# Optimization experiments

Measured on AMD Instinct MI355X. Metric: run time of the kernel, lower is better.

## Reference

```python
import jax, jax.numpy as jnp
import numpy as np

N = 512        # input image side (== n after rounding, cor = n//2)
N_DET = 512
N_SPAN = 3
N_ANGLES_INIT = 1024
BATCH = 16
C = 1


def _splineB3(x2, r):
    sizex = len(x2)
    x2 = x2 - (x2[-1] + x2[0]) / 2
    stepx = x2[1] - x2[0]
    ri = int(np.ceil(2 * r))
    r = r * stepx
    c = int(np.ceil((sizex + 1) / 2.0))
    x2c = x2[c - 1]
    x = x2[c - ri - 1:c + ri]
    d = np.abs(x - x2c) / r
    B3 = np.zeros_like(x)
    for ix in range(-ri, ri + 1):
        i = ix + ri
        if d[i] < 1:
            B3[i] = (3 * d[i] ** 3 - 6 * d[i] ** 2 + 4) / 6
        elif d[i] < 2:
            B3[i] = (-d[i] ** 3 + 6 * d[i] ** 2 - 12 * d[i] + 8) / 6
    B3f = np.zeros_like(x2)
    B3f[c - ri - 1:c + ri] = B3
    return B3f


def _precompute():
    beta = np.pi / N_SPAN
    n = N  # ceil((512+0)/16)*16 == 512 since cor == n//2
    n_det = N_DET
    os_angles = int(max(round(3.0 * n / 2 / N_ANGLES_INIT), 1))  # == 1
    n_angles = os_angles * N_ANGLES_INIT
    angles = np.arange(n_angles) * np.pi / n_angles - beta / 2
    s = np.linspace(-1, 1, n_det)
    a_R = np.sin(beta / 2) / (1 + np.sin(beta / 2))
    a_m = (np.cos(beta / 2) - np.sin(beta / 2)) / (1 + np.sin(beta / 2))
    t = np.linspace(-np.pi / 2, np.pi / 2, 1000)
    w = a_R * np.cos(t) + (1 - a_R) + 1j * a_R * np.sin(t)
    g = np.nanmax(np.log(np.abs(w)) + np.log(np.cos(beta / 2 - np.arctan2(w.imag, w.real))))
    n_th = n_det
    n_rho = 2 * n_det
    d_th = 2 * beta / n_th
    d_rho = (g - np.log(a_m)) / n_rho
    th_lp = np.arange(-n_th / 2, n_th / 2) * d_th
    rho_lp = np.arange(-n_rho, 0) * d_rho
    b3_th = np.fft.fft(np.fft.ifftshift(_splineB3(th_lp, 1)))
    b3_rho = np.fft.fft(np.fft.ifftshift(_splineB3(rho_lp, 1)))
    b3_com = np.outer(b3_rho, b3_th)
    # ---- zeta coefficients (vectorized over k_rho) ----
    n_th_large = 4 * n_th
    k_rho = np.arange(-n_rho / 2, n_rho / 2, dtype='float32')
    th_sp_large = np.arange(-n_th_large / 2, n_th_large / 2) / n_th_large * beta * 2
    h = np.ones(n_th_large)
    correcting = 1 + np.array([-216254335, 679543284, -1412947389, 2415881496, -3103579086,
                               2939942400, -2023224114, 984515304, -321455811, 63253516,
                               -5675265]) / 958003200.0
    correcting[0] = 2 * (correcting[0] - 0.5)
    h[0] *= correcting[0]
    for j in range(1, len(correcting)):
        h[j] *= correcting[j]
        h[-j] *= correcting[j]
    expo = -2 * np.pi * 1j * k_rho / (g - np.log(a_m)) - 1
    fcosa = np.cos(th_sp_large)[None, :].astype('complex128') ** expo[:, None]
    fZ = np.fft.fftshift(np.fft.fft(np.fft.fftshift(h[None, :] * fcosa, axes=-1), axis=-1), axes=-1)
    fZ = fZ[:, n_th_large // 2 - n_th // 2: n_th_large // 2 + n_th // 2] * (th_sp_large[1] - th_sp_large[0])
    fZ[0] = 0
    fZ[:, 0] = 0
    zeta = np.fft.fftshift(fZ)
    const = np.sqrt(n_det * os_angles / n_angles) * np.pi / 4 / a_R / np.sqrt(2)
    zeta = zeta[:, :n_th // 2 + 1] * const
    zeta = zeta / b3_com[:, :n_th // 2 + 1]  # cubic interp prefilter compensation
    # ---- cartesian -> log-polar gather indices (floor, per span) ----
    tmp1 = np.outer(np.exp(rho_lp), np.cos(th_lp)).flatten()
    tmp2 = np.outer(np.exp(rho_lp), np.sin(th_lp)).flatten()
    idx_lp2c = []
    for k in range(N_SPAN):
        a = k * beta + beta / 2
        l1 = ((tmp1 - (1 - a_R)) * np.cos(a) - tmp2 * np.sin(a)) / a_R
        l2 = -(((tmp1 - (1 - a_R)) * np.sin(a) + tmp2 * np.cos(a)) / a_R)
        l1 = (l1 + 1) / 2 * (n_det - 1)
        l2 = (l2 + 1) / 2 * (n_det - 1)
        y = np.clip(np.floor(l1), 0, n_det - 2).astype(np.int32)
        x = np.clip(np.floor(l2), 0, n_det - 2).astype(np.int32)
        idx_lp2c.append(y * n_det + x)
    # ---- log-polar -> (angle, det) gather indices + span masks ----
    s0, th0 = np.meshgrid(s, angles)
    th0 = th0.flatten()
    s0 = s0.flatten()
    width_2 = n_angles * n_det // n_rho  # == n_th with these dims
    idx_p2lp = []
    pids = []
    with np.errstate(all='ignore'):
        for k in range(N_SPAN):
            pids.append(((th0 >= k * beta - beta / 2) & (th0 < k * beta + beta / 2)).astype(np.float32))
            th00 = th0 - k * beta
            p1 = (th00 - th_lp[0]) / (th_lp[-1] - th_lp[0]) * (n_th - 1)
            p2 = np.nan_to_num(np.log(s0 * a_R + (1 - a_R) * np.cos(th00)))
            p2 = (p2 - rho_lp[0]) / (rho_lp[-1] - rho_lp[0]) * (n_rho - 1)
            y = np.clip(np.floor(p2), 0, n_rho - 2).astype(np.int64)
            x = np.clip(np.floor(p1), 0, width_2 - 2).astype(np.int64)
            idx_p2lp.append((y * width_2 + x).astype(np.int32))
    return dict(
        n_rho=n_rho, n_th=n_th, n_angles=n_angles, n_det=n_det,
        zeta=jnp.asarray(zeta.astype(np.complex64)),
        e_rho=jnp.asarray(np.exp(rho_lp).astype(np.float32)).reshape(1, -1, 1, 1),
        idx_lp2c=jnp.asarray(np.stack(idx_lp2c)),
        idx_p2lp=jnp.asarray(np.stack(idx_p2lp)),
        pids=jnp.asarray(np.stack(pids)),
    )

_CONST = _precompute()


def setup_inputs() -> dict:
    key = jax.random.key(0)
    x = jax.random.normal(key, (BATCH, N, N, C), dtype=jnp.float32)
    return {"x": x}


def reference(x):
    c = _CONST
    b = x.shape[0]
    n_rho, n_th = c["n_rho"], c["n_th"]
    flat = x.reshape(b, N * N, C)
    out = jnp.zeros((b, c["n_angles"] * c["n_det"], C), dtype=x.dtype)
    for k in range(N_SPAN):
        # gather cartesian image onto log-polar grid (floor sampling)
        lp = flat[:, c["idx_lp2c"][k], :].reshape(b, n_rho, n_th, C) * c["e_rho"]
        # FFT-domain convolution with zeta kernel
        F = jnp.fft.rfft2(lp, axes=(1, 2)) * c["zeta"][None, :, :, None]
        gk = jnp.fft.irfft2(F, s=(n_rho, n_th), axes=(1, 2)).astype(x.dtype)
        # gather back onto (angle, detector) grid, masked by span membership
        samp = gk.reshape(b, n_rho * n_th, C)[:, c["idx_p2lp"][k], :]
        out = out + c["pids"][k][None, :, None] * samp
    return out.reshape(b, c["n_angles"], c["n_det"], C)
```

## Files before the change

kernel.cpp:

```cpp
#include <hip/hip_runtime.h>
#include <cmath>

#ifndef M_PI
#define M_PI 3.14159265358979323846
#endif

#define NIMG 512
#define NRHO 1024
#define NTH  512
#define ZROWS 256
#define GROWS 256
#define S4   520
#define PTOT (1024*512)
#define NSPAN 3

struct Consts { double G_LA, d_rho, aR, dth, constv; };

static Consts compute_consts() {
  Consts c;
  const double beta = M_PI / 3.0;
  const double sb = sin(beta / 2.0), cb = cos(beta / 2.0);
  const double aR = sb / (1.0 + sb);
  const double am = (cb - sb) / (1.0 + sb);
  double g = -1e300;
  const double start = -M_PI / 2.0, stop = M_PI / 2.0;
  const double delta = (stop - start) / 999.0;
  for (int i = 0; i < 1000; ++i) {
    double t = (i == 999) ? stop : (double)i * delta + start;
    double wre = aR * cos(t) + (1.0 - aR);
    double wim = aR * sin(t);
    double v = log(hypot(wre, wim)) + log(cos(beta / 2.0 - atan2(wim, wre)));
    if (!std::isnan(v) && v > g) g = v;
  }
  c.aR    = aR;
  c.G_LA  = g - log(am);
  c.d_rho = c.G_LA / 1024.0;
  double t1 = (-1023.0 / 2048.0) * beta * 2.0;
  double t0 = (-1024.0 / 2048.0) * beta * 2.0;
  c.dth = t1 - t0;
  c.constv = sqrt(0.5) * M_PI / 4.0 / aR / sqrt(2.0);
  return c;
}
static const Consts g_C = compute_consts();

__device__ __forceinline__ float2 cmulf(float2 a, float2 b) {
  return make_float2(a.x * b.x - a.y * b.y, a.x * b.y + a.y * b.x);
}
__device__ __forceinline__ float2 cmulcf(float2 a, float2 w) {
  return make_float2(a.x * w.x + a.y * w.y, a.y * w.x - a.x * w.y);
}
__device__ __forceinline__ int SW(int i) { return i ^ ((i >> 5) & 31); }
__device__ __forceinline__ int PD(int i) { return i + (i >> 4); }
__device__ __forceinline__ int dr4_10(int v) {
  int r = 0;
  #pragma unroll
  for (int k = 0; k < 5; ++k) { r = (r << 2) | (v & 3); v >>= 2; }
  return r;
}
__device__ __forceinline__ double h_val(int jj) {
  const double ctab[11] = {-216254335.0, 679543284.0, -1412947389.0, 2415881496.0,
                           -3103579086.0, 2939942400.0, -2023224114.0, 984515304.0,
                           -321455811.0, 63253516.0, -5675265.0};
  int j = -1;
  if (jj <= 10) j = jj;
  else if (jj >= 2038) j = 2048 - jj;
  if (j < 0) return 1.0;
  double c = 1.0 + ctab[j] / 958003200.0;
  if (j == 0) c = 2.0 * (c - 0.5);
  return c;
}

__global__ __launch_bounds__(256) void k_pre(double* __restrict__ Ltab,
                                             double* __restrict__ amp,
                                             float2* __restrict__ tw1024f,
                                             float2* __restrict__ tw2048f) {
  int id = blockIdx.x * 256 + threadIdx.x;
  const double beta = M_PI / 3.0;
  if (id < 2048) {
    double th = ((double)(id - 1024) / 2048.0) * beta * 2.0;
    double L = log(cos(th));
    Ltab[id] = L;
    amp[id]  = h_val(id) * exp(-L);
  }
  if (id < 1024) {
    double a1 = -2.0 * M_PI * (double)id / 1024.0;
    double a2 = -2.0 * M_PI * (double)id / 2048.0;
    double s1, c1, s2, c2;
    sincos(a1, &s1, &c1); sincos(a2, &s2, &c2);
    tw1024f[id] = make_float2((float)c1, (float)s1);
    tw2048f[id] = make_float2((float)c2, (float)s2);
  }
}

__global__ __launch_bounds__(256) void k_zeta(const double* __restrict__ Ltab,
                                              const double* __restrict__ amp,
                                              const float2* __restrict__ tw2048f,
                                              float2* __restrict__ zetaT,
                                              double G_LA, double dth, double constv) {
  __shared__ float2 s[2048 + 128];
  __shared__ float2 twl[1024 + 64];
  const int i   = blockIdx.x;
  const int tid = threadIdx.x;
  for (int e = tid; e < 1024; e += 256) twl[PD(e)] = tw2048f[e];
  const double om = 2.0 * M_PI * (double)(i - 512) / G_LA;
  const double INV2PI = 1.0 / (2.0 * M_PI);
  for (int j = tid; j < 2048; j += 256) {
    int jj = (j + 1024) & 2047;
    double ph = -om * Ltab[jj] * INV2PI;
    ph -= floor(ph);
    float ang = (float)ph * 6.28318530717958647f;
    float sv, cv; __sincosf(ang, &sv, &cv);
    float a = (float)amp[jj];
    s[PD(__brev((unsigned)j) >> 21)] = make_float2(a * cv, a * sv);
  }
  for (int lh = 0; lh < 11; ++lh) {
    __syncthreads();
    for (int e = tid; e < 1024; e += 256) {
      int pos = e & ((1 << lh) - 1);
      int ia  = ((e >> lh) << (lh + 1)) | pos;
      float2 w = twl[PD(pos << (10 - lh))];
      float2 u = s[PD(ia)];
      float2 v = cmulf(s[PD(ia + (1 << lh))], w);
      s[PD(ia)]             = make_float2(u.x + v.x, u.y + v.y);
      s[PD(ia + (1 << lh))] = make_float2(u.x - v.x, u.y - v.y);
    }
  }
  __syncthreads();
  const int i2 = (i + 512) & 1023;
  const int p  = dr4_10(i2);
  const double b3r = (4.0 + 2.0 * cos(2.0 * M_PI * (double)i2 / 1024.0)) / 6.0;
  if (tid < 256) {
    int j2 = tid;
    float2 z = make_float2(0.f, 0.f);
    if (i != 0) {
      float2 F = s[PD(j2)];
      double b3t = (4.0 + 2.0 * cos(2.0 * M_PI * (double)j2 / 512.0)) / 6.0;
      double sc = dth * constv / (b3r * b3t) * (1.0 / (1024.0 * 512.0));
      z = make_float2((float)((double)F.x * sc), (float)((double)F.y * sc));
    }
    zetaT[(size_t)j2 * 1024 + p] = z;
  }
}

__global__ __launch_bounds__(256) void k_idx_lp2c(int* __restrict__ idx1,
                                                  double d_rho, double aR) {
  int q = blockIdx.x * 256 + threadIdx.x;
  int span = q >> 19;
  int ql = q & (NRHO * NTH - 1);
  int i = ql >> 9, j = ql & 511;
  const double beta = M_PI / 3.0;
  double d_th = 2.0 * beta / 512.0;
  double th = (double)(j - 256) * d_th;
  double er = exp((double)(i - 1024) * d_rho);
  double t1 = er * cos(th), t2 = er * sin(th);
  double a = (double)span * beta + beta / 2.0;
  double ca = cos(a), sa = sin(a);
  double l1 = ((t1 - (1.0 - aR)) * ca - t2 * sa) / aR;
  double l2 = -(((t1 - (1.0 - aR)) * sa + t2 * ca) / aR);
  l1 = (l1 + 1.0) / 2.0 * 511.0;
  l2 = (l2 + 1.0) / 2.0 * 511.0;
  double fy = floor(l1); fy = fy < 0.0 ? 0.0 : (fy > 510.0 ? 510.0 : fy);
  double fx = floor(l2); fx = fx < 0.0 ? 0.0 : (fx > 510.0 ? 510.0 : fx);
  idx1[q] = (int)fy * 512 + (int)fx;
}

__global__ __launch_bounds__(256) void k_gather_rfft(const float* __restrict__ x,
                                                     const int* __restrict__ idx1,
                                                     const float2* __restrict__ tw1024f,
                                                     float2* __restrict__ T,
                                                     int b0, double d_rho) {
  __shared__ float2 s[4][S4];
  __shared__ float2 twl[256];
  const int bx   = blockIdx.x;
  const int g    = ((bx & 7) << 4) | (bx >> 3);
  const int i0   = g * 8;
  const int lb   = blockIdx.y;
  const int span = blockIdx.z;
  const int tid  = threadIdx.x;
  twl[tid] = tw1024f[2 * tid];
  const int r  = tid >> 5;
  const int t5 = tid & 31;
  const float er = (float)exp((double)(i0 + r - 1024) * d_rho);
  const float* xb = x + (size_t)(b0 + lb) * (NIMG * NIMG);
  const int4* ip = (const int4*)(idx1 + span * (NRHO * NTH) + (i0 + r) * 512 + t5 * 16);
  int4 i4[4];
  #pragma unroll
  for (int u = 0; u < 4; ++u) i4[u] = ip[u];
  float v[16];
  #pragma unroll
  for (int u = 0; u < 4; ++u) {
    v[4 * u + 0] = xb[i4[u].x];
    v[4 * u + 1] = xb[i4[u].y];
    v[4 * u + 2] = xb[i4[u].z];
    v[4 * u + 3] = xb[i4[u].w];
  }
  float* sm = (float*)s[r >> 1];
  const int p = r & 1;
  #pragma unroll
  for (int u = 0; u < 16; ++u) {
    int j = t5 * 16 + u;
    int slot = __brev((unsigned)j) >> 23;
    sm[2 * SW(slot) + p] = v[u] * er;
  }
  #pragma unroll
  for (int lh = 0; lh < 8; lh += 2) {
    __syncthreads();
    const int q = 1 << lh;
    #pragma unroll
    for (int it = 0; it < 2; ++it) {
      int e = tid + (it << 8);
      int m = e >> 7, gq = e & 127;
      int pos = gq & (q - 1);
      int base = ((gq >> lh) << (lh + 2)) | pos;
      float2 w1 = twl[pos << (8 - lh)];
      float2 w2 = twl[pos << (7 - lh)];
      float2* smm = s[m];
      float2 a = smm[SW(base)];
      float2 b = smm[SW(base + q)];
      float2 c = smm[SW(base + 2 * q)];
      float2 d = smm[SW(base + 3 * q)];
      float2 wb = cmulf(b, w1), wd = cmulf(d, w1);
      float2 t0 = make_float2(a.x + wb.x, a.y + wb.y);
      float2 t1 = make_float2(a.x - wb.x, a.y - wb.y);
      float2 t2 = make_float2(c.x + wd.x, c.y + wd.y);
      float2 t3 = make_float2(c.x - wd.x, c.y - wd.y);
      float2 z2 = cmulf(t2, w2);
      float2 p3 = cmulf(t3, w2);
      float2 z3 = make_float2(p3.y, -p3.x);
      smm[SW(base)]         = make_float2(t0.x + z2.x, t0.y + z2.y);
      smm[SW(base + 2 * q)] = make_float2(t0.x - z2.x, t0.y - z2.y);
      smm[SW(base + q)]     = make_float2(t1.x + z3.x, t1.y + z3.y);
      smm[SW(base + 3 * q)] = make_float2(t1.x - z3.x, t1.y - z3.y);
    }
  }
  __syncthreads();
  #pragma unroll
  for (int it = 0; it < 4; ++it) {
    int e = tid + (it << 8);
    int m = e >> 8, b = e & 255;
    float2 w = twl[b];
    float2* smm = s[m];
    float2 u = smm[SW(b)];
    float2 vv = cmulf(smm[SW(b + 256)], w);
    smm[SW(b)]       = make_float2(u.x + vv.x, u.y + vv.y);
    smm[SW(b + 256)] = make_float2(u.x - vv.x, u.y - vv.y);
  }
  __syncthreads();
  float2* Tb = T + (size_t)(span * gridDim.y + lb) * (ZROWS * NRHO);
  for (int it = 0; it < 8; ++it) {
    int e = tid + (it << 8);
    int k = e >> 3, rr = e & 7;
    int m = rr >> 1, pp = rr & 1;
    float2 Z  = s[m][SW(k)];
    float2 Zc = s[m][SW((512 - k) & 511)];
    float2 F;
    if (!pp) F = make_float2(0.5f * (Z.x + Zc.x), 0.5f * (Z.y - Zc.y));
    else     F = make_float2(0.5f * (Z.y + Zc.y), 0.5f * (Zc.x - Z.x));
    Tb[(size_t)k * NRHO + i0 + rr] = F;
  }
}

__global__ __launch_bounds__(256) void k_fft_rho(float2* __restrict__ T,
                                                 const float2* __restrict__ zetaT,
                                                 const float2* __restrict__ tw1024f) {
  __shared__ float2 s[2][1024 + 64];
  __shared__ float2 twl[1024 + 64];
  const int j0   = blockIdx.x * 2;
  const int lb   = blockIdx.y;
  const int span = blockIdx.z;
  const int tid  = threadIdx.x;
  for (int e = tid; e < 1024; e += 256) twl[PD(e)] = tw1024f[e];
  float2* row0 = T + ((size_t)(span * gridDim.y + lb) * ZROWS + j0) * NRHO;
  #pragma unroll
  for (int m = 0; m < 2; ++m) {
    const float4* rp = (const float4*)(row0 + (size_t)m * NRHO);
    for (int e = tid; e < 512; e += 256) {
      float4 v = rp[e];
      s[m][PD(2 * e)]     = make_float2(v.x, v.y);
      s[m][PD(2 * e + 1)] = make_float2(v.z, v.w);
    }
  }
  __syncthreads();
  #pragma unroll
  for (int lq = 8; lq >= 0; lq -= 2) {
    const int q = 1 << lq, tfac = 256 >> lq;
    int jj = tid & (q - 1);
    int base = ((tid >> lq) << (lq + 2)) | jj;
    int t1i = jj * tfac;
    float2 w1 = twl[PD(t1i)], w2 = twl[PD(2 * t1i)], w3 = twl[PD(3 * t1i)];
    #pragma unroll
    for (int m = 0; m < 2; ++m) {
      float2* sm = s[m];
      float2 a = sm[PD(base)], b = sm[PD(base + q)];
      float2 c = sm[PD(base + 2 * q)], d = sm[PD(base + 3 * q)];
      float2 A = make_float2(a.x + c.x, a.y + c.y);
      float2 C = make_float2(a.x - c.x, a.y - c.y);
      float2 B = make_float2(b.x + d.x, b.y + d.y);
      float2 D = make_float2(b.x - d.x, b.y - d.y);
      float2 u0 = make_float2(A.x + B.x, A.y + B.y);
      float2 u2 = make_float2(A.x - B.x, A.y - B.y);
      float2 u1 = make_float2(C.x + D.y, C.y - D.x);
      float2 u3 = make_float2(C.x - D.y, C.y + D.x);
      sm[PD(base)]         = u0;
      sm[PD(base + q)]     = cmulf(u1, w1);
      sm[PD(base + 2 * q)] = cmulf(u2, w2);
      sm[PD(base + 3 * q)] = cmulf(u3, w3);
    }
    __syncthreads();
  }
  #pragma unroll
  for (int m = 0; m < 2; ++m) {
    const float2* zrow = zetaT + (size_t)(j0 + m) * NRHO;
    for (int e = tid; e < 1024; e += 256)
      s[m][PD(e)] = cmulf(s[m][PD(e)], zrow[e]);
  }
  __syncthreads();
  #pragma unroll
  for (int lq = 0; lq <= 8; lq += 2) {
    const int q = 1 << lq, tfac = 256 >> lq;
    int jj = tid & (q - 1);
    int base = ((tid >> lq) << (lq + 2)) | jj;
    int t1i = jj * tfac;
    float2 w1 = twl[PD(t1i)], w2 = twl[PD(2 * t1i)], w3 = twl[PD(3 * t1i)];
    #pragma unroll
    for (int m = 0; m < 2; ++m) {
      float2* sm = s[m];
      float2 u0 = sm[PD(base)];
      float2 u1 = cmulcf(sm[PD(base + q)],     w1);
      float2 u2 = cmulcf(sm[PD(base + 2 * q)], w2);
      float2 u3 = cmulcf(sm[PD(base + 3 * q)], w3);
      float2 t0 = make_float2(u0.x + u2.x, u0.y + u2.y);
      float2 t1 = make_float2(u0.x - u2.x, u0.y - u2.y);
      float2 t2 = make_float2(u1.x + u3.x, u1.y + u3.y);
      float2 t3 = make_float2(u1.x - u3.x, u1.y - u3.y);
      sm[PD(base)]         = make_float2(t0.x + t2.x, t0.y + t2.y);
      sm[PD(base + 2 * q)] = make_float2(t0.x - t2.x, t0.y - t2.y);
      sm[PD(base + q)]     = make_float2(t1.x - t3.y, t1.y + t3.x);
      sm[PD(base + 3 * q)] = make_float2(t1.x + t3.y, t1.y - t3.x);
    }
    __syncthreads();
  }
  #pragma unroll
  for (int m = 0; m < 2; ++m) {
    float4* rp = (float4*)(row0 + (size_t)m * NRHO);
    for (int e = tid; e < 512; e += 256) {
      float2 a = s[m][PD(2 * e)], b = s[m][PD(2 * e + 1)];
      rp[e] = make_float4(a.x, a.y, b.x, b.y);
    }
  }
}

__global__ __launch_bounds__(256) void k_irfft_th(const float2* __restrict__ T,
                                                  const float2* __restrict__ tw1024f,
                                                  float* __restrict__ gkT) {
  __shared__ float2 s[4][S4];
  __shared__ float2 twl[256];
  const int i0   = blockIdx.x * 8;
  const int lb   = blockIdx.y;
  const int span = blockIdx.z;
  const int tid  = threadIdx.x;
  twl[tid] = tw1024f[2 * tid];
  const float2* Tb = T + (size_t)(span * gridDim.y + lb) * (ZROWS * NRHO);
  __syncthreads();
  for (int it = 0; it < 8; ++it) {
    int e = tid + (it << 8);
    int k = e >> 3, rr = e & 7;
    int m = rr >> 1, p = rr & 1;
    s[m][SW(k + 256 * p)] = Tb[(size_t)k * NRHO + i0 + rr];
  }
  __syncthreads();
  float2 Zr[8];
  for (int it = 0; it < 8; ++it) {
    int e = tid + (it << 8);
    int m = e >> 9, k = e & 511;
    float2 z;
    if (k == 256) z = make_float2(0.f, 0.f);
    else {
      int k2 = (k < 256) ? k : 512 - k;
      float2 F0 = s[m][SW(k2)];
      float2 F1 = s[m][SW(256 + k2)];
      if (k2 == 0) { F0.y = 0.f; F1.y = 0.f; }
      if (k < 256) z = make_float2(F0.x - F1.y, F0.y + F1.x);
      else         z = make_float2(F0.x + F1.y, F1.x - F0.y);
    }
    Zr[it] = z;
  }
  __syncthreads();
  for (int it = 0; it < 8; ++it) {
    int e = tid + (it << 8);
    int m = e >> 9, k = e & 511;
    s[m][SW(k)] = Zr[it];
  }
  #pragma unroll
  for (int lh = 8; lh >= 2; lh -= 2) {
    __syncthreads();
    const int h = 1 << (lh - 1);
    #pragma unroll
    for (int it = 0; it < 2; ++it) {
      int e = tid + (it << 8);
      int m = e >> 7, gq = e & 127;
      int pos = gq & (h - 1);
      int base = ((gq >> (lh - 1)) << (lh + 1)) | pos;
      float2 wa = twl[pos << (8 - lh)];
      float2 w2 = twl[pos << (9 - lh)];
      float2* sm = s[m];
      float2 a = sm[SW(base)];
      float2 b = sm[SW(base + h)];
      float2 c = sm[SW(base + 2 * h)];
      float2 d = sm[SW(base + 3 * h)];
      float2 ap = make_float2(a.x + c.x, a.y + c.y);
      float2 cp = cmulcf(make_float2(a.x - c.x, a.y - c.y), wa);
      float2 bp = make_float2(b.x + d.x, b.y + d.y);
      float2 tt = cmulcf(make_float2(b.x - d.x, b.y - d.y), wa);
      float2 dp = make_float2(-tt.y, tt.x);
      sm[SW(base)]         = make_float2(ap.x + bp.x, ap.y + bp.y);
      sm[SW(base + h)]     = cmulcf(make_float2(ap.x - bp.x, ap.y - bp.y), w2);
      sm[SW(base + 2 * h)] = make_float2(cp.x + dp.x, cp.y + dp.y);
      sm[SW(base + 3 * h)] = cmulcf(make_float2(cp.x - dp.x, cp.y - dp.y), w2);
    }
  }
  __syncthreads();
  #pragma unroll
  for (int it = 0; it < 4; ++it) {
    int e = tid + (it << 8);
    int m = e >> 8, b = e & 255;
    int ia = b << 1;
    float2* sm = s[m];
    float2 u = sm[SW(ia)];
    float2 v = sm[SW(ia + 1)];
    sm[SW(ia)]     = make_float2(u.x + v.x, u.y + v.y);
    sm[SW(ia + 1)] = make_float2(u.x - v.x, u.y - v.y);
  }
  __syncthreads();
  float* gb = gkT + (size_t)(span * gridDim.y + lb) * (GROWS * NRHO);
  for (int it = 0; it < 8; ++it) {
    int e = tid + (it << 8);
    int ro = e >> 3, rr = e & 7;
    int j = ro + 128;
    int jslot = __brev((unsigned)j) >> 23;
    float2 z = s[rr >> 1][SW(jslot)];
    gb[(size_t)ro * NRHO + i0 + rr] = (rr & 1) ? z.y : z.x;
  }
}

__global__ __launch_bounds__(256) void k_scatter(const float* __restrict__ gkT,
                                                 float* __restrict__ out,
                                                 int b0, int chunk,
                                                 double d_rho, double aR) {
  int p = blockIdx.x * 256 + threadIdx.x;
  if (p >= PTOT) return;
  const int t = p >> 9;
  const int d = p & 511;
  const int span = (3 * t) >> 10;
  const double beta = M_PI / 3.0;
  double th0 = (double)t * M_PI / 1024.0 - beta / 2.0;
  double th00 = th0 - (double)span * beta;
  double d_th = 2.0 * beta / 512.0;
  double th_lp0 = -256.0 * d_th, th_lpL = 255.0 * d_th;
  double p1 = (th00 - th_lp0) / (th_lpL - th_lp0) * 511.0;
  double s0v = (d == 511) ? 1.0 : (double)d * (2.0 / 511.0) - 1.0;
  double p2 = log(s0v * aR + (1.0 - aR) * cos(th00));
  double rho0 = -1024.0 * d_rho, rhoL = -1.0 * d_rho;
  p2 = (p2 - rho0) / (rhoL - rho0) * 1023.0;
  double fy = floor(p2); fy = fy < 0.0 ? 0.0 : (fy > 1022.0 ? 1022.0 : fy);
  double fx = floor(p1); fx = fx < 0.0 ? 0.0 : (fx > 510.0 ? 510.0 : fx);
  int idx = ((int)fx - 128) * 1024 + (int)fy;
  const float* gsp = gkT + (size_t)span * chunk * (GROWS * NRHO);
  for (int lb = 0; lb < chunk; ++lb)
    out[(size_t)(b0 + lb) * PTOT + p] = gsp[(size_t)lb * (GROWS * NRHO) + idx];
}

extern "C" void kernel_launch(void* const* d_in, const int* in_sizes, int n_in,
                              void* d_out, int out_size, void* d_ws, size_t ws_size,
                              hipStream_t stream) {
  (void)n_in; (void)out_size;
  const float* x = (const float*)d_in[0];
  float* out = (float*)d_out;
  const int batch = in_sizes[0] / (NIMG * NIMG);

  const size_t zeta_b = (size_t)ZROWS * NRHO * sizeof(float2);
  const size_t idx_b  = (size_t)NSPAN * NRHO * NTH * sizeof(int);
  const size_t tab_b  = 2048 * sizeof(double) * 2 + 1024 * sizeof(float2) * 2;
  const size_t per_b  = (size_t)NSPAN * ((size_t)ZROWS * NRHO * sizeof(float2)
                      + (size_t)GROWS * NRHO * sizeof(float));
  int chunk = batch;
  while (chunk > 1 && zeta_b + idx_b + tab_b + (size_t)chunk * per_b > ws_size) chunk >>= 1;

  char* ws = (char*)d_ws;
  float2* zetaT   = (float2*)ws;  ws += zeta_b;
  int*    idx1    = (int*)ws;     ws += idx_b;
  double* Ltab    = (double*)ws;  ws += 2048 * sizeof(double);
  double* amp     = (double*)ws;  ws += 2048 * sizeof(double);
  float2* tw1024f = (float2*)ws;  ws += 1024 * sizeof(float2);
  float2* tw2048f = (float2*)ws;  ws += 1024 * sizeof(float2);
  float2* T       = (float2*)ws;  ws += (size_t)NSPAN * chunk * ZROWS * NRHO * sizeof(float2);
  float*  gkT     = (float*)ws;

  k_pre     <<<dim3(8),    dim3(256), 0, stream>>>(Ltab, amp, tw1024f, tw2048f);
  k_zeta    <<<dim3(1024), dim3(256), 0, stream>>>(Ltab, amp, tw2048f, zetaT,
                                                   g_C.G_LA, g_C.dth, g_C.constv);
  k_idx_lp2c<<<dim3((NSPAN * NRHO * NTH) / 256), dim3(256), 0, stream>>>(idx1, g_C.d_rho, g_C.aR);

  for (int b0 = 0; b0 < batch; b0 += chunk) {
    int c = (b0 + chunk <= batch) ? chunk : (batch - b0);
    k_gather_rfft<<<dim3(NRHO / 8, c, NSPAN), dim3(256), 0, stream>>>(x, idx1, tw1024f, T, b0, g_C.d_rho);
    k_fft_rho    <<<dim3(ZROWS / 2, c, NSPAN), dim3(256), 0, stream>>>(T, zetaT, tw1024f);
    k_irfft_th   <<<dim3(NRHO / 8, c, NSPAN), dim3(256), 0, stream>>>(T, tw1024f, gkT);
    k_scatter    <<<dim3(PTOT / 256), dim3(256), 0, stream>>>(gkT, out, b0, c,
                                                              g_C.d_rho, g_C.aR);
  }
}
```

Measured before the change: 283.9 us.

## Rewrite rho-axis FFT as register-resident radix-16 passes, four rows per block

The 1024-point rho FFT/zeta/inverse FFT kernel now handles four rows per block, with 64 threads per row. Each thread keeps 16 elements in registers and does two radix-4 stages per pass, so shared-memory round trips and barriers drop from about five per direction to three. The final radix-4 stage is fused with the zeta multiply and the first inverse stage. The zeta table is stored in a permuted order to match the new output ordering. Per-thread register use rises, which may lower occupancy, and the grid has half as many blocks.

After: 262.4 us. 7.6% less time.

```diff
diff --git a/kernel.cpp b/kernel.cpp
--- a/kernel.cpp
+++ b/kernel.cpp
@@ -56,6 +56,28 @@
   #pragma unroll
   for (int k = 0; k < 5; ++k) { r = (r << 2) | (v & 3); v >>= 2; }
   return r;
+}
+__device__ __forceinline__ void bf4f(float2 a, float2 b, float2 c, float2 d,
+                                     float2& y0, float2& y1, float2& y2, float2& y3) {
+  float2 A = make_float2(a.x + c.x, a.y + c.y);
+  float2 C = make_float2(a.x - c.x, a.y - c.y);
+  float2 B = make_float2(b.x + d.x, b.y + d.y);
+  float2 D = make_float2(b.x - d.x, b.y - d.y);
+  y0 = make_float2(A.x + B.x, A.y + B.y);
+  y2 = make_float2(A.x - B.x, A.y - B.y);
+  y1 = make_float2(C.x + D.y, C.y - D.x);
+  y3 = make_float2(C.x - D.y, C.y + D.x);
+}
+__device__ __forceinline__ void bf4i(float2 u0, float2 u1, float2 u2, float2 u3,
+                                     float2& z0, float2& z1, float2& z2, float2& z3) {
+  float2 t0 = make_float2(u0.x + u2.x, u0.y + u2.y);
+  float2 t1 = make_float2(u0.x - u2.x, u0.y - u2.y);
+  float2 t2 = make_float2(u1.x + u3.x, u1.y + u3.y);
+  float2 t3 = make_float2(u1.x - u3.x, u1.y - u3.y);
+  z0 = make_float2(t0.x + t2.x, t0.y + t2.y);
+  z2 = make_float2(t0.x - t2.x, t0.y - t2.y);
+  z1 = make_float2(t1.x - t3.y, t1.y + t3.x);
+  z3 = make_float2(t1.x + t3.y, t1.y - t3.x);
 }
 __device__ __forceinline__ double h_val(int jj) {
   const double ctab[11] = {-216254335.0, 679543284.0, -1412947389.0, 2415881496.0,
@@ -128,6 +150,7 @@
   __syncthreads();
   const int i2 = (i + 512) & 1023;
   const int p  = dr4_10(i2);
+  const int pp = ((p & 15) << 6) | (p >> 4);
   const double b3r = (4.0 + 2.0 * cos(2.0 * M_PI * (double)i2 / 1024.0)) / 6.0;
   if (tid < 256) {
     int j2 = tid;
@@ -138,7 +161,7 @@
       double sc = dth * constv / (b3r * b3t) * (1.0 / (1024.0 * 512.0));
       z = make_float2((float)((double)F.x * sc), (float)((double)F.y * sc));
     }
-    zetaT[(size_t)j2 * 1024 + p] = z;
+    zetaT[(size_t)j2 * 1024 + pp] = z;
   }
 }
 
@@ -263,91 +286,165 @@
 __global__ __launch_bounds__(256) void k_fft_rho(float2* __restrict__ T,
                                                  const float2* __restrict__ zetaT,
                                                  const float2* __restrict__ tw1024f) {
-  __shared__ float2 s[2][1024 + 64];
+  __shared__ float2 s[4][1024 + 64];
   __shared__ float2 twl[1024 + 64];
-  const int j0   = blockIdx.x * 2;
+  const int j0   = blockIdx.x * 4;
   const int lb   = blockIdx.y;
   const int span = blockIdx.z;
   const int tid  = threadIdx.x;
+  const int bin  = tid >> 6;
+  const int t6   = tid & 63;
+  float2* rowb = T + ((size_t)(span * gridDim.y + lb) * ZROWS + j0 + bin) * NRHO;
+
+  float2 r[4][4];
+  #pragma unroll
+  for (int c = 0; c < 4; ++c)
+    #pragma unroll
+    for (int a = 0; a < 4; ++a)
+      r[c][a] = rowb[t6 + 64 * a + 256 * c];
+
   for (int e = tid; e < 1024; e += 256) twl[PD(e)] = tw1024f[e];
-  float2* row0 = T + ((size_t)(span * gridDim.y + lb) * ZROWS + j0) * NRHO;
-  #pragma unroll
-  for (int m = 0; m < 2; ++m) {
-    const float4* rp = (const float4*)(row0 + (size_t)m * NRHO);
-    for (int e = tid; e < 512; e += 256) {
-      float4 v = rp[e];
-      s[m][PD(2 * e)]     = make_float2(v.x, v.y);
-      s[m][PD(2 * e + 1)] = make_float2(v.z, v.w);
-    }
-  }
-  __syncthreads();
-  #pragma unroll
-  for (int lq = 8; lq >= 0; lq -= 2) {
-    const int q = 1 << lq, tfac = 256 >> lq;
-    int jj = tid & (q - 1);
-    int base = ((tid >> lq) << (lq + 2)) | jj;
-    int t1i = jj * tfac;
-    float2 w1 = twl[PD(t1i)], w2 = twl[PD(2 * t1i)], w3 = twl[PD(3 * t1i)];
-    #pragma unroll
-    for (int m = 0; m < 2; ++m) {
-      float2* sm = s[m];
-      float2 a = sm[PD(base)], b = sm[PD(base + q)];
-      float2 c = sm[PD(base + 2 * q)], d = sm[PD(base + 3 * q)];
-      float2 A = make_float2(a.x + c.x, a.y + c.y);
-      float2 C = make_float2(a.x - c.x, a.y - c.y);
-      float2 B = make_float2(b.x + d.x, b.y + d.y);
-      float2 D = make_float2(b.x - d.x, b.y - d.y);
-      float2 u0 = make_float2(A.x + B.x, A.y + B.y);
-      float2 u2 = make_float2(A.x - B.x, A.y - B.y);
-      float2 u1 = make_float2(C.x + D.y, C.y - D.x);
-      float2 u3 = make_float2(C.x - D.y, C.y + D.x);
-      sm[PD(base)]         = u0;
-      sm[PD(base + q)]     = cmulf(u1, w1);
-      sm[PD(base + 2 * q)] = cmulf(u2, w2);
-      sm[PD(base + 3 * q)] = cmulf(u3, w3);
-    }
-    __syncthreads();
-  }
-  #pragma unroll
-  for (int m = 0; m < 2; ++m) {
-    const float2* zrow = zetaT + (size_t)(j0 + m) * NRHO;
-    for (int e = tid; e < 1024; e += 256)
-      s[m][PD(e)] = cmulf(s[m][PD(e)], zrow[e]);
-  }
-  __syncthreads();
-  #pragma unroll
-  for (int lq = 0; lq <= 8; lq += 2) {
-    const int q = 1 << lq, tfac = 256 >> lq;
-    int jj = tid & (q - 1);
-    int base = ((tid >> lq) << (lq + 2)) | jj;
-    int t1i = jj * tfac;
-    float2 w1 = twl[PD(t1i)], w2 = twl[PD(2 * t1i)], w3 = twl[PD(3 * t1i)];
-    #pragma unroll
-    for (int m = 0; m < 2; ++m) {
-      float2* sm = s[m];
-      float2 u0 = sm[PD(base)];
-      float2 u1 = cmulcf(sm[PD(base + q)],     w1);
-      float2 u2 = cmulcf(sm[PD(base + 2 * q)], w2);
-      float2 u3 = cmulcf(sm[PD(base + 3 * q)], w3);
-      float2 t0 = make_float2(u0.x + u2.x, u0.y + u2.y);
-      float2 t1 = make_float2(u0.x - u2.x, u0.y - u2.y);
-      float2 t2 = make_float2(u1.x + u3.x, u1.y + u3.y);
-      float2 t3 = make_float2(u1.x - u3.x, u1.y - u3.y);
-      sm[PD(base)]         = make_float2(t0.x + t2.x, t0.y + t2.y);
-      sm[PD(base + 2 * q)] = make_float2(t0.x - t2.x, t0.y - t2.y);
-      sm[PD(base + q)]     = make_float2(t1.x - t3.y, t1.y + t3.x);
-      sm[PD(base + 3 * q)] = make_float2(t1.x + t3.y, t1.y - t3.x);
-    }
-    __syncthreads();
-  }
-  #pragma unroll
-  for (int m = 0; m < 2; ++m) {
-    float4* rp = (float4*)(row0 + (size_t)m * NRHO);
-    for (int e = tid; e < 512; e += 256) {
-      float2 a = s[m][PD(2 * e)], b = s[m][PD(2 * e + 1)];
-      rp[e] = make_float4(a.x, a.y, b.x, b.y);
-    }
-  }
+  __syncthreads();
+
+  #pragma unroll
+  for (int a = 0; a < 4; ++a) {
+    int jj = t6 + 64 * a;
+    float2 y0, y1, y2, y3;
+    bf4f(r[0][a], r[1][a], r[2][a], r[3][a], y0, y1, y2, y3);
+    r[0][a] = y0;
+    r[1][a] = cmulf(y1, twl[PD(jj)]);
+    r[2][a] = cmulf(y2, twl[PD(2 * jj)]);
+    r[3][a] = cmulf(y3, twl[PD(3 * jj)]);
+  }
+  {
+    float2 w1 = twl[PD(4 * t6)], w2 = twl[PD(8 * t6)], w3 = twl[PD(12 * t6)];
+    #pragma unroll
+    for (int c = 0; c < 4; ++c) {
+      float2 y0, y1, y2, y3;
+      bf4f(r[c][0], r[c][1], r[c][2], r[c][3], y0, y1, y2, y3);
+      r[c][0] = y0; r[c][1] = cmulf(y1, w1); r[c][2] = cmulf(y2, w2); r[c][3] = cmulf(y3, w3);
+    }
+  }
+  #pragma unroll
+  for (int c = 0; c < 4; ++c)
+    #pragma unroll
+    for (int a = 0; a < 4; ++a)
+      s[bin][PD(t6 + 64 * a + 256 * c)] = r[c][a];
+  __syncthreads();
+
+  const int B64 = t6 >> 2, b2 = t6 & 3;
+  const int fbase = 64 * B64 + b2;
+  #pragma unroll
+  for (int c = 0; c < 4; ++c)
+    #pragma unroll
+    for (int a = 0; a < 4; ++a)
+      r[c][a] = s[bin][PD(fbase + 4 * a + 16 * c)];
+  #pragma unroll
+  for (int a = 0; a < 4; ++a) {
+    int ji = 16 * (b2 + 4 * a);
+    float2 y0, y1, y2, y3;
+    bf4f(r[0][a], r[1][a], r[2][a], r[3][a], y0, y1, y2, y3);
+    r[0][a] = y0;
+    r[1][a] = cmulf(y1, twl[PD(ji)]);
+    r[2][a] = cmulf(y2, twl[PD(2 * ji)]);
+    r[3][a] = cmulf(y3, twl[PD(3 * ji)]);
+  }
+  {
+    float2 w1 = twl[PD(64 * b2)], w2 = twl[PD(128 * b2)], w3 = twl[PD(192 * b2)];
+    #pragma unroll
+    for (int c = 0; c < 4; ++c) {
+      float2 y0, y1, y2, y3;
+      bf4f(r[c][0], r[c][1], r[c][2], r[c][3], y0, y1, y2, y3);
+      r[c][0] = y0; r[c][1] = cmulf(y1, w1); r[c][2] = cmulf(y2, w2); r[c][3] = cmulf(y3, w3);
+    }
+  }
+  #pragma unroll
+  for (int c = 0; c < 4; ++c)
+    #pragma unroll
+    for (int a = 0; a < 4; ++a)
+      s[bin][PD(fbase + 4 * a + 16 * c)] = r[c][a];
+  __syncthreads();
+
+  {
+    const float2* zp = zetaT + (size_t)(j0 + bin) * NRHO;
+    #pragma unroll
+    for (int u = 0; u < 4; ++u) {
+      int o0 = 16 * t6 + 4 * u;
+      float2 a0 = s[bin][PD(o0)],     a1 = s[bin][PD(o0 + 1)];
+      float2 a2 = s[bin][PD(o0 + 2)], a3 = s[bin][PD(o0 + 3)];
+      float2 y0, y1, y2, y3;
+      bf4f(a0, a1, a2, a3, y0, y1, y2, y3);
+      float2 q0 = zp[64 * (4 * u + 0) + t6];
+      float2 q1 = zp[64 * (4 * u + 1) + t6];
+      float2 q2 = zp[64 * (4 * u + 2) + t6];
+      float2 q3 = zp[64 * (4 * u + 3) + t6];
+      y0 = cmulf(y0, q0); y1 = cmulf(y1, q1); y2 = cmulf(y2, q2); y3 = cmulf(y3, q3);
+      float2 z0, z1, z2, z3;
+      bf4i(y0, y1, y2, y3, z0, z1, z2, z3);
+      s[bin][PD(o0)]     = z0; s[bin][PD(o0 + 1)] = z1;
+      s[bin][PD(o0 + 2)] = z2; s[bin][PD(o0 + 3)] = z3;
+    }
+  }
+  __syncthreads();
+
+  #pragma unroll
+  for (int c = 0; c < 4; ++c)
+    #pragma unroll
+    for (int a = 0; a < 4; ++a)
+      r[c][a] = s[bin][PD(fbase + 4 * a + 16 * c)];
+  {
+    float2 w1 = twl[PD(64 * b2)], w2 = twl[PD(128 * b2)], w3 = twl[PD(192 * b2)];
+    #pragma unroll
+    for (int c = 0; c < 4; ++c) {
+      float2 u1 = cmulcf(r[c][1], w1);
+      float2 u2 = cmulcf(r[c][2], w2);
+      float2 u3 = cmulcf(r[c][3], w3);
+      bf4i(r[c][0], u1, u2, u3, r[c][0], r[c][1], r[c][2], r[c][3]);
+    }
+  }
+  #pragma unroll
+  for (int a = 0; a < 4; ++a) {
+    int ji = 16 * (b2 + 4 * a);
+    float2 u1 = cmulcf(r[1][a], twl[PD(ji)]);
+    float2 u2 = cmulcf(r[2][a], twl[PD(2 * ji)]);
+    float2 u3 = cmulcf(r[3][a], twl[PD(3 * ji)]);
+    bf4i(r[0][a], u1, u2, u3, r[0][a], r[1][a], r[2][a], r[3][a]);
+  }
+  #pragma unroll
+  for (int c = 0; c < 4; ++c)
+    #pragma unroll
+    for (int a = 0; a < 4; ++a)
+      s[bin][PD(fbase + 4 * a + 16 * c)] = r[c][a];
+  __syncthreads();
+
+  #pragma unroll
+  for (int c = 0; c < 4; ++c)
+    #pragma unroll
+    for (int a = 0; a < 4; ++a)
+      r[c][a] = s[bin][PD(t6 + 64 * a + 256 * c)];
+  {
+    float2 w1 = twl[PD(4 * t6)], w2 = twl[PD(8 * t6)], w3 = twl[PD(12 * t6)];
+    #pragma unroll
+    for (int c = 0; c < 4; ++c) {
+      float2 u1 = cmulcf(r[c][1], w1);
+      float2 u2 = cmulcf(r[c][2], w2);
+      float2 u3 = cmulcf(r[c][3], w3);
+      bf4i(r[c][0], u1, u2, u3, r[c][0], r[c][1], r[c][2], r[c][3]);
+    }
+  }
+  #pragma unroll
+  for (int a = 0; a < 4; ++a) {
+    int jj = t6 + 64 * a;
+    float2 u1 = cmulcf(r[1][a], twl[PD(jj)]);
+    float2 u2 = cmulcf(r[2][a], twl[PD(2 * jj)]);
+    float2 u3 = cmulcf(r[3][a], twl[PD(3 * jj)]);
+    bf4i(r[0][a], u1, u2, u3, r[0][a], r[1][a], r[2][a], r[3][a]);
+  }
+  #pragma unroll
+  for (int c = 0; c < 4; ++c)
+    #pragma unroll
+    for (int a = 0; a < 4; ++a)
+      rowb[t6 + 64 * a + 256 * c] = r[c][a];
 }
 
 __global__ __launch_bounds__(256) void k_irfft_th(const float2* __restrict__ T,
@@ -504,7 +601,7 @@
   for (int b0 = 0; b0 < batch; b0 += chunk) {
     int c = (b0 + chunk <= batch) ? chunk : (batch - b0);
     k_gather_rfft<<<dim3(NRHO / 8, c, NSPAN), dim3(256), 0, stream>>>(x, idx1, tw1024f, T, b0, g_C.d_rho);
-    k_fft_rho    <<<dim3(ZROWS / 2, c, NSPAN), dim3(256), 0, stream>>>(T, zetaT, tw1024f);
+    k_fft_rho    <<<dim3(ZROWS / 4, c, NSPAN), dim3(256), 0, stream>>>(T, zetaT, tw1024f);
     k_irfft_th   <<<dim3(NRHO / 8, c, NSPAN), dim3(256), 0, stream>>>(T, tw1024f, gkT);
     k_scatter    <<<dim3(PTOT / 256), dim3(256), 0, stream>>>(gkT, out, b0, c,
                                                               g_C.d_rho, g_C.aR);
```
